# Optimization experiments

Measured on AMD Instinct MI355X. Metric: run time of the kernel, lower is better.

Reference implementation:

```python
import jax, jax.numpy as jnp
import numpy as np
from jax import lax

N = 1024          # proposals per image
C = 81            # classes incl. background
F = 1024          # feature dim
K = 100           # detections_per_img
IMG_W, IMG_H = 1216.0, 800.0
SCORE_THRESH = 0.05
NMS_THRESH = 0.5
BBOX_CLIP = float(np.log(1000.0 / 16.0))
WX, WY, WW, WH = 10.0, 10.0, 5.0, 5.0     # BoxCoder default weights


def setup_inputs() -> dict:
    key = jax.random.key(0)
    k1, k2, k3, k4, k5 = jax.random.split(key, 5)
    class_logits = jax.random.normal(k1, (N, C), jnp.float32) * 2.0
    box_regression = jax.random.normal(k2, (N, C * 4), jnp.float32) * 0.2
    xy = jax.random.uniform(k3, (N, 2), jnp.float32) * jnp.array([IMG_W * 0.7, IMG_H * 0.7], jnp.float32)
    wh = 16.0 + jax.random.uniform(k4, (N, 2), jnp.float32) * jnp.array([IMG_W * 0.3, IMG_H * 0.3], jnp.float32)
    proposal_boxes = jnp.concatenate([xy, xy + wh], axis=1)  # valid xyxy
    features = jax.random.normal(k5, (N, F), jnp.float32)
    return {"class_logits": class_logits, "box_regression": box_regression,
            "proposal_boxes": proposal_boxes, "features": features}


def _decode(rel, boxes):
    # BoxCoder.decode with weights (10,10,5,5), TO_REMOVE=1. rel:[N,C*4] boxes:[N,4] -> [N,C,4]
    rel = rel.reshape(N, C, 4)
    widths = boxes[:, 2] - boxes[:, 0] + 1.0
    heights = boxes[:, 3] - boxes[:, 1] + 1.0
    ctr_x = boxes[:, 0] + 0.5 * widths
    ctr_y = boxes[:, 1] + 0.5 * heights
    dx = rel[..., 0] / WX
    dy = rel[..., 1] / WY
    dw = jnp.minimum(rel[..., 2] / WW, BBOX_CLIP)
    dh = jnp.minimum(rel[..., 3] / WH, BBOX_CLIP)
    pcx = dx * widths[:, None] + ctr_x[:, None]
    pcy = dy * heights[:, None] + ctr_y[:, None]
    pw = jnp.exp(dw) * widths[:, None]
    ph = jnp.exp(dh) * heights[:, None]
    return jnp.stack([pcx - 0.5 * pw, pcy - 0.5 * ph,
                      pcx + 0.5 * pw - 1.0, pcy + 0.5 * ph - 1.0], axis=-1)


def _clip(b):
    # clip_to_image with TO_REMOVE=1
    x1 = jnp.clip(b[..., 0], 0.0, IMG_W - 1.0)
    y1 = jnp.clip(b[..., 1], 0.0, IMG_H - 1.0)
    x2 = jnp.clip(b[..., 2], 0.0, IMG_W - 1.0)
    y2 = jnp.clip(b[..., 3], 0.0, IMG_H - 1.0)
    return jnp.stack([x1, y1, x2, y2], axis=-1)


def _nms_class(boxes_c, scores_c, valid_c):
    # Sequential hard NMS for one class with fixed shapes. Invalid (below score
    # thresh) boxes can neither be kept nor suppress others.
    s_sort = jnp.where(valid_c, scores_c, -jnp.inf)
    order = jnp.argsort(-s_sort)              # descending score
    b = boxes_c[order]
    v = valid_c[order]
    s = scores_c[order]
    area = (b[:, 2] - b[:, 0] + 1.0) * (b[:, 3] - b[:, 1] + 1.0)
    lt = jnp.maximum(b[:, None, :2], b[None, :, :2])
    rb = jnp.minimum(b[:, None, 2:], b[None, :, 2:])
    whd = jnp.clip(rb - lt + 1.0, 0.0)
    inter = whd[..., 0] * whd[..., 1]
    iou = inter / (area[:, None] + area[None, :] - inter)  # [N,N]
    idx = jnp.arange(N)
    def body(i, keep):
        sup = (iou[i] > NMS_THRESH) & keep[i] & (idx > i)
        return keep & ~sup
    keep = lax.fori_loop(0, N, body, v)
    return b, order, jnp.where(keep, s, -1.0)


def reference(class_logits, box_regression, proposal_boxes, features):
    probs = jax.nn.softmax(class_logits, axis=-1)          # [N,C]
    dec = _clip(_decode(box_regression, proposal_boxes))    # [N,C,4]
    boxes_cls = jnp.transpose(dec[:, 1:, :], (1, 0, 2))     # [C-1,N,4] (skip background)
    scores_cls = probs[:, 1:].T                             # [C-1,N]
    valid = scores_cls > SCORE_THRESH
    b_s, order, s_kept = jax.vmap(_nms_class)(boxes_cls, scores_cls, valid)
    flat_s = s_kept.reshape(-1)                             # [(C-1)*N]
    top_s, top_i = lax.top_k(flat_s, K)
    cls_i = top_i // N
    pos_i = top_i % N
    boxes_out = b_s[cls_i, pos_i]                           # [K,4]
    orig = order[cls_i, pos_i]                              # original proposal idx
    feat_out = features[orig]                               # [K,F]
    labels = cls_i + 1
    ok = top_s > 0.0
    scores_out = jnp.where(ok, top_s, 0.0)
    boxes_out = jnp.where(ok[:, None], boxes_out, 0.0)
    feat_out = jnp.where(ok[:, None], feat_out, 0.0)
    labels = jnp.where(ok, labels, 0)
    return boxes_out, scores_out, feat_out, labels
```

## Files before the change

### kernel.cpp

```cpp
#include <hip/hip_runtime.h>
#include <math.h>

#define N 1024
#define C 81
#define F 1024
#define K 100
#define NC1 80
#define MAXC (NC1 * N)
#define HBASE 0x3D00
#define HSIZE 1024
#define SELCAP 2048

#define SCORE_THRESH 0.05f
#define NMS_THRESH   0.5f
#define BBOX_CLIP    4.135166556742356f
#define IMG_W1       1215.0f
#define IMG_H1       799.0f

typedef unsigned long long u64;
typedef unsigned int u32;

__device__ float4 decode_box(const float* __restrict__ pboxes,
                             const float* __restrict__ boxreg, int idx, int cl)
{
    float4 pb = ((const float4*)pboxes)[idx];
    float4 r  = *(const float4*)(boxreg + (size_t)idx * (C * 4) + cl * 4);
    float w  = pb.z - pb.x + 1.0f, h = pb.w - pb.y + 1.0f;
    float cx = pb.x + 0.5f * w,  cy = pb.y + 0.5f * h;
    float dx = r.x / 10.0f, dy = r.y / 10.0f;
    float dw = fminf(r.z / 5.0f, BBOX_CLIP);
    float dh = fminf(r.w / 5.0f, BBOX_CLIP);
    float pcx = dx * w + cx, pcy = dy * h + cy;
    float pw = expf(dw) * w, ph = expf(dh) * h;
    float x1 = pcx - 0.5f * pw,        y1 = pcy - 0.5f * ph;
    float x2 = pcx + 0.5f * pw - 1.0f, y2 = pcy + 0.5f * ph - 1.0f;
    x1 = fminf(fmaxf(x1, 0.0f), IMG_W1);
    y1 = fminf(fmaxf(y1, 0.0f), IMG_H1);
    x2 = fminf(fmaxf(x2, 0.0f), IMG_W1);
    y2 = fminf(fmaxf(y2, 0.0f), IMG_H1);
    return make_float4(x1, y1, x2, y2);
}

__global__ __launch_bounds__(256) void k_softmax(
    const float* __restrict__ logits, float2* __restrict__ ms,
    int* __restrict__ hist, int* __restrict__ counter)
{
    int gid = blockIdx.x * 256 + threadIdx.x;
    if (gid < HSIZE) hist[gid] = 0;
    if (gid == 0) *counter = 0;

    int n = blockIdx.x * 4 + (threadIdx.x >> 6);
    int t = threadIdx.x & 63;

    float v1 = logits[n * C + t];
    float v2 = (t < C - 64) ? logits[n * C + 64 + t] : -INFINITY;
    float m = fmaxf(v1, v2);
    for (int off = 32; off; off >>= 1) m = fmaxf(m, __shfl_xor(m, off));
    float e1 = expf(v1 - m);
    float e2 = (t < C - 64) ? expf(v2 - m) : 0.0f;
    float s = e1 + e2;
    for (int off = 32; off; off >>= 1) s += __shfl_xor(s, off);

    if (t == 0) ms[n] = make_float2(m, s);
}

__global__ __launch_bounds__(256) void k_class(
    const float* __restrict__ logits, const float* __restrict__ boxreg,
    const float* __restrict__ pboxes, const float2* __restrict__ ms,
    u64* __restrict__ ckey, float4* __restrict__ cbox, int* __restrict__ corig,
    int* __restrict__ hist, int* __restrict__ counter)
{
    int c = blockIdx.x;
    int cl = c + 1;
    int t = threadIdx.x;
    int lane = t & 63, wv = t >> 6;

    __shared__ u64    skey64[N];
    __shared__ float4 sbox[N];
    __shared__ float  sarea[N];
    __shared__ int    skeep[N];
    __shared__ u64    sup[256][4];
    __shared__ u64    skw[4];
    __shared__ int    swc[4];

    float2 p0 = ms[t],       p1 = ms[t + 256];
    float2 p2 = ms[t + 512], p3 = ms[t + 768];
    float s0 = expf(logits[(t      ) * C + cl] - p0.x) / p0.y;
    float s1 = expf(logits[(t + 256) * C + cl] - p1.x) / p1.y;
    float s2 = expf(logits[(t + 512) * C + cl] - p2.x) / p2.y;
    float s3 = expf(logits[(t + 768) * C + cl] - p3.x) / p3.y;
    int f0 = s0 > SCORE_THRESH, f1 = s1 > SCORE_THRESH;
    int f2 = s2 > SCORE_THRESH, f3 = s3 > SCORE_THRESH;

    u64 lmask = (1ull << lane) - 1ull;
    u64 b0 = __ballot(f0), b1 = __ballot(f1);
    u64 b2 = __ballot(f2), b3 = __ballot(f3);
    int wcount = __popcll(b0) + __popcll(b1) + __popcll(b2) + __popcll(b3);
    if (lane == 0) swc[wv] = wcount;
    __syncthreads();
    int w0c = swc[0], w1c = swc[1], w2c = swc[2], w3c = swc[3];
    int V = w0c + w1c + w2c + w3c;
    int wbase = (wv > 0 ? w0c : 0) + (wv > 1 ? w1c : 0) + (wv > 2 ? w2c : 0);
    {
        int o0 = wbase;
        int o1 = o0 + __popcll(b0);
        int o2 = o1 + __popcll(b1);
        int o3 = o2 + __popcll(b2);
        if (f0) skey64[o0 + __popcll(b0 & lmask)] =
            ((u64)__float_as_uint(s0) << 32) | (u32)~(u32)(t);
        if (f1) skey64[o1 + __popcll(b1 & lmask)] =
            ((u64)__float_as_uint(s1) << 32) | (u32)~(u32)(t + 256);
        if (f2) skey64[o2 + __popcll(b2 & lmask)] =
            ((u64)__float_as_uint(s2) << 32) | (u32)~(u32)(t + 512);
        if (f3) skey64[o3 + __popcll(b3 & lmask)] =
            ((u64)__float_as_uint(s3) << 32) | (u32)~(u32)(t + 768);
    }
    __syncthreads();
    if (V == 0) return;

    if (V <= 64) {
        if (t < 64) {
            u64 key = (lane < V) ? skey64[lane] : 0ull;
            for (int k = 2; k <= 64; k <<= 1) {
                for (int j = k >> 1; j > 0; j >>= 1) {
                    u64 other = __shfl_xor(key, j);
                    bool takeMax = (((lane & j) == 0) == ((lane & k) == 0));
                    bool gt = key > other;
                    key = (takeMax == gt) ? key : other;
                }
            }
            bool act = key != 0ull;
            float4 b = make_float4(0.f, 0.f, 0.f, 0.f);
            float area = 0.0f;
            if (act) {
                int idx = (int)(~(u32)(key & 0xffffffffu));
                b = decode_box(pboxes, boxreg, idx, cl);
                area = (b.z - b.x + 1.0f) * (b.w - b.y + 1.0f);
                cbox[c * N + lane]  = b;
                corig[c * N + lane] = idx;
            }
            int kept = act ? 1 : 0;
            for (int i = 0; i + 1 < V; ++i) {
                int   ki  = __shfl(kept, i);
                float bix = __shfl(b.x, i), biy = __shfl(b.y, i);
                float biz = __shfl(b.z, i), biw = __shfl(b.w, i);
                float ai  = __shfl(area, i);
                if (ki && lane > i && kept) {
                    float lx = fmaxf(bix, b.x), ly = fmaxf(biy, b.y);
                    float rx = fminf(biz, b.z), ry = fminf(biw, b.w);
                    float ww = fmaxf(rx - lx + 1.0f, 0.0f);
                    float hh = fmaxf(ry - ly + 1.0f, 0.0f);
                    float inter = ww * hh;
                    float iou = inter / (ai + area - inter);
                    if (iou > NMS_THRESH) kept = 0;
                }
            }
            if (kept) {
                int pos = atomicAdd(counter, 1);
                u32 sb = (u32)(key >> 32);
                ckey[pos] = ((u64)sb << 32) | (u64)(u32)~(u32)(c * N + lane);
                atomicAdd(&hist[(int)(sb >> 16) - HBASE], 1);
            }
        }
        return;
    }

    if (V <= 256) {
        int P = 128;
        while (P < V) P <<= 1;
        for (int i = V + t; i < P; i += 256) skey64[i] = 0ull;
        __syncthreads();
        for (int k = 2; k <= P; k <<= 1) {
            for (int j = k >> 1; j > 0; j >>= 1) {
                if (t < P) {
                    int i = t, ixj = i ^ j;
                    if (ixj > i) {
                        u64 a = skey64[i], bb = skey64[ixj];
                        bool desc = ((i & k) == 0);
                        if (desc ? (a < bb) : (a > bb)) { skey64[i] = bb; skey64[ixj] = a; }
                    }
                }
                __syncthreads();
            }
        }
        for (int p = t; p < V; p += 256) {
            int idx = (int)(~(u32)(skey64[p] & 0xffffffffu));
            float4 b = decode_box(pboxes, boxreg, idx, cl);
            sbox[p]  = b;
            sarea[p] = (b.z - b.x + 1.0f) * (b.w - b.y + 1.0f);
            cbox[c * N + p]  = b;
            corig[c * N + p] = idx;
        }
        __syncthreads();
        for (int i = t; i < V; i += 256) {
            float4 bi = sbox[i];
            float  ai = sarea[i];
            u64 w[4] = {0ull, 0ull, 0ull, 0ull};
            #pragma unroll
            for (int g = 0; g < 4; ++g) {
                int jlo = (i + 1 > g * 64) ? i + 1 : g * 64;
                int jhi = (V < (g + 1) * 64) ? V : (g + 1) * 64;
                for (int j = jlo; j < jhi; ++j) {
                    float4 bj = sbox[j];
                    float lx = fmaxf(bi.x, bj.x), ly = fmaxf(bi.y, bj.y);
                    float rx = fminf(bi.z, bj.z), ry = fminf(bi.w, bj.w);
                    float ww = fmaxf(rx - lx + 1.0f, 0.0f);
                    float hh = fmaxf(ry - ly + 1.0f, 0.0f);
                    float inter = ww * hh;
                    float iou = inter / (ai + sarea[j] - inter);
                    if (iou > NMS_THRESH) w[g] |= 1ull << (j & 63);
                }
            }
            sup[i][0] = w[0]; sup[i][1] = w[1];
            sup[i][2] = w[2]; sup[i][3] = w[3];
        }
        __syncthreads();
        if (t < 64) {
            u64 r0w0 = sup[t][0], r0w1 = sup[t][1], r0w2 = sup[t][2], r0w3 = sup[t][3];
            u64 r1w1 = 0, r1w2 = 0, r1w3 = 0;
            u64 r2w2 = 0, r2w3 = 0;
            u64 r3w3 = 0;
            if (64 + t < V)  { r1w1 = sup[64 + t][1];  r1w2 = sup[64 + t][2];  r1w3 = sup[64 + t][3]; }
            if (128 + t < V) { r2w2 = sup[128 + t][2]; r2w3 = sup[128 + t][3]; }
            if (192 + t < V) { r3w3 = sup[192 + t][3]; }
            u64 k0 = ~0ull, k1 = ~0ull, k2 = ~0ull, k3 = ~0ull;
            {
                int lim = (V < 64) ? V : 64;
                for (int i = 0; i < lim; ++i)
                    if ((k0 >> i) & 1) {
                        k0 &= ~__shfl(r0w0, i); k1 &= ~__shfl(r0w1, i);
                        k2 &= ~__shfl(r0w2, i); k3 &= ~__shfl(r0w3, i);
                    }
            }
            if (V > 64) {
                int lim = (V - 64 < 64) ? V - 64 : 64;
                for (int i = 0; i < lim; ++i)
                    if ((k1 >> i) & 1) {
                        k1 &= ~__shfl(r1w1, i);
                        k2 &= ~__shfl(r1w2, i); k3 &= ~__shfl(r1w3, i);
                    }
            }
            if (V > 128) {
                int lim = (V - 128 < 64) ? V - 128 : 64;
                for (int i = 0; i < lim; ++i)
                    if ((k2 >> i) & 1) {
                        k2 &= ~__shfl(r2w2, i); k3 &= ~__shfl(r2w3, i);
                    }
            }
            if (V > 192) {
                int lim = V - 192;
                for (int i = 0; i < lim; ++i)
                    if ((k3 >> i) & 1) k3 &= ~__shfl(r3w3, i);
            }
            if (t == 0) { skw[0] = k0; skw[1] = k1; skw[2] = k2; skw[3] = k3; }
        }
        __syncthreads();
        for (int p = t; p < V; p += 256) {
            if ((skw[p >> 6] >> (p & 63)) & 1ull) {
                int pos = atomicAdd(counter, 1);
                u32 sb = (u32)(skey64[p] >> 32);
                ckey[pos] = ((u64)sb << 32) | (u64)(u32)~(u32)(c * N + p);
                atomicAdd(&hist[(int)(sb >> 16) - HBASE], 1);
            }
        }
        return;
    }

    {
        int P = 512;
        while (P < V) P <<= 1;
        for (int i = V + t; i < P; i += 256) skey64[i] = 0ull;
        __syncthreads();
        for (int k = 2; k <= P; k <<= 1) {
            for (int j = k >> 1; j > 0; j >>= 1) {
                for (int i = t; i < P; i += 256) {
                    int ixj = i ^ j;
                    if (ixj > i) {
                        u64 a = skey64[i], bb = skey64[ixj];
                        bool desc = ((i & k) == 0);
                        if (desc ? (a < bb) : (a > bb)) { skey64[i] = bb; skey64[ixj] = a; }
                    }
                }
                __syncthreads();
            }
        }
        for (int p = t; p < V; p += 256) {
            int idx = (int)(~(u32)(skey64[p] & 0xffffffffu));
            float4 b = decode_box(pboxes, boxreg, idx, cl);
            sbox[p]  = b;
            sarea[p] = (b.z - b.x + 1.0f) * (b.w - b.y + 1.0f);
            skeep[p] = 1;
            cbox[c * N + p]  = b;
            corig[c * N + p] = idx;
        }
        __syncthreads();
        for (int i = 0; i < V; ++i) {
            if (skeep[i]) {
                float4 bi = sbox[i];
                float  ai = sarea[i];
                for (int j = i + 1 + t; j < V; j += 256) {
                    if (skeep[j]) {
                        float4 bj = sbox[j];
                        float lx = fmaxf(bi.x, bj.x), ly = fmaxf(bi.y, bj.y);
                        float rx = fminf(bi.z, bj.z), ry = fminf(bi.w, bj.w);
                        float ww = fmaxf(rx - lx + 1.0f, 0.0f);
                        float hh = fmaxf(ry - ly + 1.0f, 0.0f);
                        float inter = ww * hh;
                        float iou = inter / (ai + sarea[j] - inter);
                        if (iou > NMS_THRESH) skeep[j] = 0;
                    }
                }
            }
            __syncthreads();
        }
        for (int p = t; p < V; p += 256) {
            if (skeep[p]) {
                int pos = atomicAdd(counter, 1);
                u32 sb = (u32)(skey64[p] >> 32);
                ckey[pos] = ((u64)sb << 32) | (u64)(u32)~(u32)(c * N + p);
                atomicAdd(&hist[(int)(sb >> 16) - HBASE], 1);
            }
        }
    }
}

__global__ __launch_bounds__(1024) void k_select(
    const int* __restrict__ counter, u64* ckey, const int* __restrict__ hist,
    float* __restrict__ sel_score, int* __restrict__ sel_flat)
{
    int t = threadIdx.x;
    int lane = t & 63, wv = t >> 6;
    __shared__ u64 keys[SELCAP];
    __shared__ int swsum[16];
    __shared__ int sb_bstar, scount;
    __shared__ u64 wk[16];
    __shared__ int wp[16];

    int M = *counter;
    if (t == 0) { sb_bstar = 0; scount = 0; }

    int lsum = hist[t];
    int v = lsum;
    #pragma unroll
    for (int off = 1; off < 64; off <<= 1) {
        int o = __shfl_down(v, off);
        if (lane + off < 64) v += o;
    }
    if (lane == 0) swsum[wv] = v;
    __syncthreads();
    if (t < 64) {
        int w = (t < 16) ? swsum[t] : 0;
        #pragma unroll
        for (int off = 1; off < 16; off <<= 1) {
            int o = __shfl_down(w, off);
            if (t + off < 16) w += o;
        }
        if (t < 16) swsum[t] = w;
    }
    __syncthreads();
    int higher = (wv < 15) ? swsum[wv + 1] : 0;
    int base = v + higher - lsum;
    if (base < K && base + lsum >= K) sb_bstar = t;
    __syncthreads();
    int bstar = sb_bstar;

    for (int p = t; p < M; p += 1024) {
        u64 kk = ckey[p];
        int b = (int)((kk >> 48) & 0xFFFF) - HBASE;
        if (b >= bstar) {
            int pos = atomicAdd(&scount, 1);
            if (pos < SELCAP) keys[pos] = kk;
        }
    }
    __syncthreads();
    int cnt = scount;

    if (cnt > SELCAP) {
        for (int k = 0; k < K; ++k) {
            u64 key = 0ull; int pos = -1;
            for (int p = t; p < M; p += 1024) {
                u64 kk = ckey[p];
                if (kk > key) { key = kk; pos = p; }
            }
            for (int off = 32; off; off >>= 1) {
                u64 ok2 = __shfl_down(key, off);
                int op = __shfl_down(pos, off);
                if (ok2 > key) { key = ok2; pos = op; }
            }
            if ((t & 63) == 0) { wk[t >> 6] = key; wp[t >> 6] = pos; }
            __syncthreads();
            if (t == 0) {
                for (int w = 1; w < 16; ++w)
                    if (wk[w] > key) { key = wk[w]; pos = wp[w]; }
                if (key != 0ull) {
                    sel_score[k] = __uint_as_float((u32)(key >> 32));
                    sel_flat[k]  = (int)(~(u32)(key & 0xffffffffu));
                    ckey[pos] = 0ull;
                } else { sel_score[k] = 0.0f; sel_flat[k] = 0; }
            }
            __syncthreads();
        }
        return;
    }

    int P = 128;
    while (P < cnt) P <<= 1;
    for (int i = cnt + t; i < P; i += 1024) keys[i] = 0ull;
    __syncthreads();

    if (P <= 1024) {
        u64 key = (t < P) ? keys[t] : 0ull;
        for (int k = 2; k <= P; k <<= 1) {
            for (int j = k >> 1; j > 0; j >>= 1) {
                if (j >= 64) {
                    if (t < P) keys[t] = key;
                    __syncthreads();
                    if (t < P) {
                        u64 other = keys[t ^ j];
                        bool takeMax = (((t & j) == 0) == ((t & k) == 0));
                        bool gt = key > other;
                        key = (takeMax == gt) ? key : other;
                    }
                    __syncthreads();
                } else {
                    u64 other = __shfl_xor(key, j);
                    bool takeMax = (((t & j) == 0) == ((t & k) == 0));
                    bool gt = key > other;
                    if (t < P) key = (takeMax == gt) ? key : other;
                }
            }
        }
        if (t < K) {
            sel_score[t] = __uint_as_float((u32)(key >> 32));
            sel_flat[t]  = (int)(~(u32)(key & 0xffffffffu));
        }
        return;
    }

    for (int k = 2; k <= P; k <<= 1) {
        for (int j = k >> 1; j > 0; j >>= 1) {
            for (int i = t; i < P; i += 1024) {
                int ixj = i ^ j;
                if (ixj > i) {
                    u64 a = keys[i], b = keys[ixj];
                    bool desc = ((i & k) == 0);
                    if (desc ? (a < b) : (a > b)) { keys[i] = b; keys[ixj] = a; }
                }
            }
            __syncthreads();
        }
    }
    if (t < K) {
        u64 key = keys[t];
        sel_score[t] = __uint_as_float((u32)(key >> 32));
        sel_flat[t]  = (int)(~(u32)(key & 0xffffffffu));
    }
}

__global__ __launch_bounds__(256) void k_gather(
    const float* __restrict__ sel_score, const int* __restrict__ sel_flat,
    const int* __restrict__ corig, const float4* __restrict__ cbox,
    const float* __restrict__ feats, float* __restrict__ out)
{
    int k = blockIdx.x, t = threadIdx.x;
    float s = sel_score[k];
    bool ok = s > 0.0f;
    float4 b = make_float4(0.f, 0.f, 0.f, 0.f);
    int label = 0, orig = 0;
    if (ok) {
        int flat = sel_flat[k];
        orig  = corig[flat];
        b     = cbox[flat];
        label = (flat >> 10) + 1;
    }
    if (t == 0) {
        out[k * 4 + 0] = b.x; out[k * 4 + 1] = b.y;
        out[k * 4 + 2] = b.z; out[k * 4 + 3] = b.w;
        out[K * 4 + k] = ok ? s : 0.0f;
        out[K * 4 + K + K * F + k] = (float)label;
    }
    const float4* src = (const float4*)(feats + (size_t)orig * F);
    float4* dst = (float4*)(out + K * 4 + K + (size_t)k * F);
    float4 z = make_float4(0.f, 0.f, 0.f, 0.f);
    if (t < F / 4) dst[t] = ok ? src[t] : z;
}

extern "C" void kernel_launch(void* const* d_in, const int* in_sizes, int n_in,
                              void* d_out, int out_size, void* d_ws, size_t ws_size,
                              hipStream_t stream)
{
    const float* logits = (const float*)d_in[0];
    const float* boxreg = (const float*)d_in[1];
    const float* pboxes = (const float*)d_in[2];
    const float* feats  = (const float*)d_in[3];
    float* out = (float*)d_out;

    char* ws = (char*)d_ws;
    size_t off = 0;
    auto alloc = [&](size_t bytes) {
        size_t cur = off;
        off = (off + bytes + 255) & ~(size_t)255;
        return cur;
    };
    u64*    ckey      = (u64*)   (ws + alloc(sizeof(u64)    * MAXC));
    float4* cbox      = (float4*)(ws + alloc(sizeof(float4) * NC1 * N));
    int*    corig     = (int*)   (ws + alloc(sizeof(int)    * NC1 * N));
    float2* ms        = (float2*)(ws + alloc(sizeof(float2) * N));
    int*    hist      = (int*)   (ws + alloc(sizeof(int)    * HSIZE));
    int*    counter   = (int*)   (ws + alloc(sizeof(int)));
    float*  sel_score = (float*) (ws + alloc(sizeof(float)  * K));
    int*    sel_flat  = (int*)   (ws + alloc(sizeof(int)    * K));

    hipLaunchKernelGGL(k_softmax, dim3(N / 4), dim3(256), 0, stream,
                       logits, ms, hist, counter);
    hipLaunchKernelGGL(k_class, dim3(NC1), dim3(256), 0, stream,
                       logits, boxreg, pboxes, ms, ckey, cbox, corig, hist, counter);
    hipLaunchKernelGGL(k_select, dim3(1), dim3(1024), 0, stream,
                       counter, ckey, hist, sel_score, sel_flat);
    hipLaunchKernelGGL(k_gather, dim3(K), dim3(256), 0, stream,
                       sel_score, sel_flat, corig, cbox, feats, out);
}
```

Baseline: 96.80 us.

## Fuse per-class NMS, top-K select and gather into one last-block kernel

Merges the class NMS, global top-K selection and feature gather kernels into a single kernel. The last block to finish, detected with an atomic done counter and threadfence, performs the histogram threshold, the sort and the gather, which removes two kernel launches and their inter-kernel gaps. The mid-size class path now runs a register and shuffle bitonic sort instead of a shared-memory sort with a barrier per step. The trade-off is that selection and gather run on one 256-thread block instead of a 1024-thread block plus 100 gather blocks, so the tail is more serialized.

```diff
diff --git a/kernel.cpp b/kernel.cpp
--- a/kernel.cpp
+++ b/kernel.cpp
@@ -43,11 +43,11 @@
 
 __global__ __launch_bounds__(256) void k_softmax(
     const float* __restrict__ logits, float2* __restrict__ ms,
-    int* __restrict__ hist, int* __restrict__ counter)
+    int* __restrict__ hist, int* __restrict__ counter, int* __restrict__ done)
 {
     int gid = blockIdx.x * 256 + threadIdx.x;
     if (gid < HSIZE) hist[gid] = 0;
-    if (gid == 0) *counter = 0;
+    if (gid == 0) { *counter = 0; *done = 0; }
 
     int n = blockIdx.x * 4 + (threadIdx.x >> 6);
     int t = threadIdx.x & 63;
@@ -64,11 +64,13 @@
     if (t == 0) ms[n] = make_float2(m, s);
 }
 
-__global__ __launch_bounds__(256) void k_class(
+__global__ __launch_bounds__(256) void k_mega(
     const float* __restrict__ logits, const float* __restrict__ boxreg,
     const float* __restrict__ pboxes, const float2* __restrict__ ms,
+    const float* __restrict__ feats,
     u64* __restrict__ ckey, float4* __restrict__ cbox, int* __restrict__ corig,
-    int* __restrict__ hist, int* __restrict__ counter)
+    int* __restrict__ hist, int* __restrict__ counter, int* __restrict__ done,
+    float* __restrict__ out)
 {
     int c = blockIdx.x;
     int cl = c + 1;
@@ -82,6 +84,15 @@
     __shared__ u64    sup[256][4];
     __shared__ u64    skw[4];
     __shared__ int    swc[4];
+    __shared__ int    sLast;
+    __shared__ int    swsum4[4];
+    __shared__ int    sbstar, scount;
+    __shared__ u64    wk[4];
+    __shared__ int    wp[4];
+    __shared__ float  ssel_score[K];
+    __shared__ int    ssel_flat[K];
+    __shared__ int    sorig[K];
+    __shared__ int    sok[K];
 
     float2 p0 = ms[t],       p1 = ms[t + 256];
     float2 p2 = ms[t + 512], p3 = ms[t + 768];
@@ -116,9 +127,8 @@
             ((u64)__float_as_uint(s3) << 32) | (u32)~(u32)(t + 768);
     }
     __syncthreads();
-    if (V == 0) return;
-
-    if (V <= 64) {
+
+    if (V > 0 && V <= 64) {
         if (t < 64) {
             u64 key = (lane < V) ? skey64[lane] : 0ull;
             for (int k = 2; k <= 64; k <<= 1) {
@@ -162,37 +172,43 @@
                 atomicAdd(&hist[(int)(sb >> 16) - HBASE], 1);
             }
         }
-        return;
-    }
-
-    if (V <= 256) {
+    } else if (V > 64 && V <= 256) {
         int P = 128;
         while (P < V) P <<= 1;
-        for (int i = V + t; i < P; i += 256) skey64[i] = 0ull;
-        __syncthreads();
+        u64 key = (t < V) ? skey64[t] : 0ull;
         for (int k = 2; k <= P; k <<= 1) {
             for (int j = k >> 1; j > 0; j >>= 1) {
-                if (t < P) {
-                    int i = t, ixj = i ^ j;
-                    if (ixj > i) {
-                        u64 a = skey64[i], bb = skey64[ixj];
-                        bool desc = ((i & k) == 0);
-                        if (desc ? (a < bb) : (a > bb)) { skey64[i] = bb; skey64[ixj] = a; }
-                    }
-                }
-                __syncthreads();
-            }
-        }
-        for (int p = t; p < V; p += 256) {
-            int idx = (int)(~(u32)(skey64[p] & 0xffffffffu));
+                if (j >= 64) {
+                    if (t < P) skey64[t] = key;
+                    __syncthreads();
+                    if (t < P) {
+                        u64 other = skey64[t ^ j];
+                        bool takeMax = (((t & j) == 0) == ((t & k) == 0));
+                        bool gt = key > other;
+                        key = (takeMax == gt) ? key : other;
+                    }
+                    __syncthreads();
+                } else {
+                    u64 other = __shfl_xor(key, j);
+                    bool takeMax = (((t & j) == 0) == ((t & k) == 0));
+                    bool gt = key > other;
+                    if (t < P) key = (takeMax == gt) ? key : other;
+                }
+            }
+        }
+        if (t < P) skey64[t] = key;
+        __syncthreads();
+        if (t < V) {
+            int idx = (int)(~(u32)(skey64[t] & 0xffffffffu));
             float4 b = decode_box(pboxes, boxreg, idx, cl);
-            sbox[p]  = b;
-            sarea[p] = (b.z - b.x + 1.0f) * (b.w - b.y + 1.0f);
-            cbox[c * N + p]  = b;
-            corig[c * N + p] = idx;
-        }
-        __syncthreads();
-        for (int i = t; i < V; i += 256) {
+            sbox[t]  = b;
+            sarea[t] = (b.z - b.x + 1.0f) * (b.w - b.y + 1.0f);
+            cbox[c * N + t]  = b;
+            corig[c * N + t] = idx;
+        }
+        __syncthreads();
+        if (t < V) {
+            int i = t;
             float4 bi = sbox[i];
             float  ai = sarea[i];
             u64 w[4] = {0ull, 0ull, 0ull, 0ull};
@@ -255,18 +271,15 @@
             if (t == 0) { skw[0] = k0; skw[1] = k1; skw[2] = k2; skw[3] = k3; }
         }
         __syncthreads();
-        for (int p = t; p < V; p += 256) {
-            if ((skw[p >> 6] >> (p & 63)) & 1ull) {
+        if (t < V) {
+            if ((skw[t >> 6] >> (t & 63)) & 1ull) {
                 int pos = atomicAdd(counter, 1);
-                u32 sb = (u32)(skey64[p] >> 32);
-                ckey[pos] = ((u64)sb << 32) | (u64)(u32)~(u32)(c * N + p);
+                u32 sb = (u32)(skey64[t] >> 32);
+                ckey[pos] = ((u64)sb << 32) | (u64)(u32)~(u32)(c * N + t);
                 atomicAdd(&hist[(int)(sb >> 16) - HBASE], 1);
             }
         }
-        return;
-    }
-
-    {
+    } else if (V > 256) {
         int P = 512;
         while (P < V) P <<= 1;
         for (int i = V + t; i < P; i += 256) skey64[i] = 0ull;
@@ -322,167 +335,160 @@
             }
         }
     }
-}
-
-__global__ __launch_bounds__(1024) void k_select(
-    const int* __restrict__ counter, u64* ckey, const int* __restrict__ hist,
-    float* __restrict__ sel_score, int* __restrict__ sel_flat)
-{
-    int t = threadIdx.x;
-    int lane = t & 63, wv = t >> 6;
-    __shared__ u64 keys[SELCAP];
-    __shared__ int swsum[16];
-    __shared__ int sb_bstar, scount;
-    __shared__ u64 wk[16];
-    __shared__ int wp[16];
-
-    int M = *counter;
-    if (t == 0) { sb_bstar = 0; scount = 0; }
-
-    int lsum = hist[t];
-    int v = lsum;
-    #pragma unroll
-    for (int off = 1; off < 64; off <<= 1) {
-        int o = __shfl_down(v, off);
-        if (lane + off < 64) v += o;
-    }
-    if (lane == 0) swsum[wv] = v;
+
+    __threadfence();
     __syncthreads();
-    if (t < 64) {
-        int w = (t < 16) ? swsum[t] : 0;
+    if (t == 0) sLast = (atomicAdd(done, 1) == NC1 - 1);
+    __syncthreads();
+    if (!sLast) return;
+    __threadfence();
+
+    {
+        int M = *counter;
+        if (t == 0) { sbstar = 0; scount = 0; }
+
+        int h0 = hist[4 * t], h1 = hist[4 * t + 1];
+        int h2 = hist[4 * t + 2], h3 = hist[4 * t + 3];
+        int gs = h0 + h1 + h2 + h3;
+        int v = gs;
         #pragma unroll
-        for (int off = 1; off < 16; off <<= 1) {
-            int o = __shfl_down(w, off);
-            if (t + off < 16) w += o;
-        }
-        if (t < 16) swsum[t] = w;
+        for (int off = 1; off < 64; off <<= 1) {
+            int o = __shfl_down(v, off);
+            if (lane + off < 64) v += o;
+        }
+        if (lane == 0) swsum4[wv] = v;
+        __syncthreads();
+        int higher = 0;
+        for (int w = wv + 1; w < 4; ++w) higher += swsum4[w];
+        int above = v + higher - gs;
+        int b3 = above, b2 = b3 + h3, b1 = b2 + h2, b0 = b1 + h1;
+        if (b0 < K && b0 + h0 >= K) sbstar = 4 * t;
+        if (b1 < K && b1 + h1 >= K) sbstar = 4 * t + 1;
+        if (b2 < K && b2 + h2 >= K) sbstar = 4 * t + 2;
+        if (b3 < K && b3 + h3 >= K) sbstar = 4 * t + 3;
+        __syncthreads();
+        int bstar = sbstar;
+
+        u64* keys = (u64*)sbox;
+        for (int p = t; p < M; p += 256) {
+            u64 kk = ckey[p];
+            int b = (int)((kk >> 48) & 0xFFFF) - HBASE;
+            if (b >= bstar) {
+                int pos = atomicAdd(&scount, 1);
+                if (pos < SELCAP) keys[pos] = kk;
+            }
+        }
+        __syncthreads();
+        int cnt = scount;
+
+        if (cnt > SELCAP) {
+            for (int k = 0; k < K; ++k) {
+                u64 key = 0ull; int pos = -1;
+                for (int p = t; p < M; p += 256) {
+                    u64 kk = ckey[p];
+                    if (kk > key) { key = kk; pos = p; }
+                }
+                for (int off = 32; off; off >>= 1) {
+                    u64 ok2 = __shfl_down(key, off);
+                    int op  = __shfl_down(pos, off);
+                    if (ok2 > key) { key = ok2; pos = op; }
+                }
+                if ((t & 63) == 0) { wk[t >> 6] = key; wp[t >> 6] = pos; }
+                __syncthreads();
+                if (t == 0) {
+                    for (int w = 1; w < 4; ++w)
+                        if (wk[w] > key) { key = wk[w]; pos = wp[w]; }
+                    if (key != 0ull) {
+                        ssel_score[k] = __uint_as_float((u32)(key >> 32));
+                        ssel_flat[k]  = (int)(~(u32)(key & 0xffffffffu));
+                        ckey[pos] = 0ull;
+                    } else { ssel_score[k] = 0.0f; ssel_flat[k] = 0; }
+                }
+                __syncthreads();
+            }
+        } else {
+            int P = 128;
+            while (P < cnt) P <<= 1;
+            for (int i = cnt + t; i < P; i += 256) keys[i] = 0ull;
+            __syncthreads();
+            if (P <= 256) {
+                u64 key = (t < P) ? keys[t] : 0ull;
+                for (int k = 2; k <= P; k <<= 1) {
+                    for (int j = k >> 1; j > 0; j >>= 1) {
+                        if (j >= 64) {
+                            if (t < P) keys[t] = key;
+                            __syncthreads();
+                            if (t < P) {
+                                u64 other = keys[t ^ j];
+                                bool takeMax = (((t & j) == 0) == ((t & k) == 0));
+                                bool gt = key > other;
+                                key = (takeMax == gt) ? key : other;
+                            }
+                            __syncthreads();
+                        } else {
+                            u64 other = __shfl_xor(key, j);
+                            bool takeMax = (((t & j) == 0) == ((t & k) == 0));
+                            bool gt = key > other;
+                            if (t < P) key = (takeMax == gt) ? key : other;
+                        }
+                    }
+                }
+                if (t < K) {
+                    ssel_score[t] = __uint_as_float((u32)(key >> 32));
+                    ssel_flat[t]  = (int)(~(u32)(key & 0xffffffffu));
+                }
+            } else {
+                for (int k = 2; k <= P; k <<= 1) {
+                    for (int j = k >> 1; j > 0; j >>= 1) {
+                        for (int i = t; i < P; i += 256) {
+                            int ixj = i ^ j;
+                            if (ixj > i) {
+                                u64 a = keys[i], b = keys[ixj];
+                                bool desc = ((i & k) == 0);
+                                if (desc ? (a < b) : (a > b)) { keys[i] = b; keys[ixj] = a; }
+                            }
+                        }
+                        __syncthreads();
+                    }
+                }
+                if (t < K) {
+                    u64 key = keys[t];
+                    ssel_score[t] = __uint_as_float((u32)(key >> 32));
+                    ssel_flat[t]  = (int)(~(u32)(key & 0xffffffffu));
+                }
+            }
+        }
     }
     __syncthreads();
-    int higher = (wv < 15) ? swsum[wv + 1] : 0;
-    int base = v + higher - lsum;
-    if (base < K && base + lsum >= K) sb_bstar = t;
-    __syncthreads();
-    int bstar = sb_bstar;
-
-    for (int p = t; p < M; p += 1024) {
-        u64 kk = ckey[p];
-        int b = (int)((kk >> 48) & 0xFFFF) - HBASE;
-        if (b >= bstar) {
-            int pos = atomicAdd(&scount, 1);
-            if (pos < SELCAP) keys[pos] = kk;
-        }
+
+    if (t < K) {
+        float s = ssel_score[t];
+        bool ok = s > 0.0f;
+        float4 b = make_float4(0.f, 0.f, 0.f, 0.f);
+        int label = 0, orig = 0;
+        if (ok) {
+            int flat = ssel_flat[t];
+            orig  = corig[flat];
+            b     = cbox[flat];
+            label = (flat >> 10) + 1;
+        }
+        sorig[t] = orig;
+        sok[t]   = ok ? 1 : 0;
+        out[t * 4 + 0] = b.x; out[t * 4 + 1] = b.y;
+        out[t * 4 + 2] = b.z; out[t * 4 + 3] = b.w;
+        out[K * 4 + t] = ok ? s : 0.0f;
+        out[K * 4 + K + K * F + t] = (float)label;
     }
     __syncthreads();
-    int cnt = scount;
-
-    if (cnt > SELCAP) {
+    {
+        float4 z = make_float4(0.f, 0.f, 0.f, 0.f);
+        float4* dstbase = (float4*)(out + K * 4 + K);
+        #pragma unroll 2
         for (int k = 0; k < K; ++k) {
-            u64 key = 0ull; int pos = -1;
-            for (int p = t; p < M; p += 1024) {
-                u64 kk = ckey[p];
-                if (kk > key) { key = kk; pos = p; }
-            }
-            for (int off = 32; off; off >>= 1) {
-                u64 ok2 = __shfl_down(key, off);
-                int op = __shfl_down(pos, off);
-                if (ok2 > key) { key = ok2; pos = op; }
-            }
-            if ((t & 63) == 0) { wk[t >> 6] = key; wp[t >> 6] = pos; }
-            __syncthreads();
-            if (t == 0) {
-                for (int w = 1; w < 16; ++w)
-                    if (wk[w] > key) { key = wk[w]; pos = wp[w]; }
-                if (key != 0ull) {
-                    sel_score[k] = __uint_as_float((u32)(key >> 32));
-                    sel_flat[k]  = (int)(~(u32)(key & 0xffffffffu));
-                    ckey[pos] = 0ull;
-                } else { sel_score[k] = 0.0f; sel_flat[k] = 0; }
-            }
-            __syncthreads();
-        }
-        return;
+            const float4* src = (const float4*)(feats + (size_t)sorig[k] * F);
+            dstbase[(size_t)k * (F / 4) + t] = sok[k] ? src[t] : z;
+        }
     }
-
-    int P = 128;
-    while (P < cnt) P <<= 1;
-    for (int i = cnt + t; i < P; i += 1024) keys[i] = 0ull;
-    __syncthreads();
-
-    if (P <= 1024) {
-        u64 key = (t < P) ? keys[t] : 0ull;
-        for (int k = 2; k <= P; k <<= 1) {
-            for (int j = k >> 1; j > 0; j >>= 1) {
-                if (j >= 64) {
-                    if (t < P) keys[t] = key;
-                    __syncthreads();
-                    if (t < P) {
-                        u64 other = keys[t ^ j];
-                        bool takeMax = (((t & j) == 0) == ((t & k) == 0));
-                        bool gt = key > other;
-                        key = (takeMax == gt) ? key : other;
-                    }
-                    __syncthreads();
-                } else {
-                    u64 other = __shfl_xor(key, j);
-                    bool takeMax = (((t & j) == 0) == ((t & k) == 0));
-                    bool gt = key > other;
-                    if (t < P) key = (takeMax == gt) ? key : other;
-                }
-            }
-        }
-        if (t < K) {
-            sel_score[t] = __uint_as_float((u32)(key >> 32));
-            sel_flat[t]  = (int)(~(u32)(key & 0xffffffffu));
-        }
-        return;
-    }
-
-    for (int k = 2; k <= P; k <<= 1) {
-        for (int j = k >> 1; j > 0; j >>= 1) {
-            for (int i = t; i < P; i += 1024) {
-                int ixj = i ^ j;
-                if (ixj > i) {
-                    u64 a = keys[i], b = keys[ixj];
-                    bool desc = ((i & k) == 0);
-                    if (desc ? (a < b) : (a > b)) { keys[i] = b; keys[ixj] = a; }
-                }
-            }
-            __syncthreads();
-        }
-    }
-    if (t < K) {
-        u64 key = keys[t];
-        sel_score[t] = __uint_as_float((u32)(key >> 32));
-        sel_flat[t]  = (int)(~(u32)(key & 0xffffffffu));
-    }
-}
-
-__global__ __launch_bounds__(256) void k_gather(
-    const float* __restrict__ sel_score, const int* __restrict__ sel_flat,
-    const int* __restrict__ corig, const float4* __restrict__ cbox,
-    const float* __restrict__ feats, float* __restrict__ out)
-{
-    int k = blockIdx.x, t = threadIdx.x;
-    float s = sel_score[k];
-    bool ok = s > 0.0f;
-    float4 b = make_float4(0.f, 0.f, 0.f, 0.f);
-    int label = 0, orig = 0;
-    if (ok) {
-        int flat = sel_flat[k];
-        orig  = corig[flat];
-        b     = cbox[flat];
-        label = (flat >> 10) + 1;
-    }
-    if (t == 0) {
-        out[k * 4 + 0] = b.x; out[k * 4 + 1] = b.y;
-        out[k * 4 + 2] = b.z; out[k * 4 + 3] = b.w;
-        out[K * 4 + k] = ok ? s : 0.0f;
-        out[K * 4 + K + K * F + k] = (float)label;
-    }
-    const float4* src = (const float4*)(feats + (size_t)orig * F);
-    float4* dst = (float4*)(out + K * 4 + K + (size_t)k * F);
-    float4 z = make_float4(0.f, 0.f, 0.f, 0.f);
-    if (t < F / 4) dst[t] = ok ? src[t] : z;
 }
 
 extern "C" void kernel_launch(void* const* d_in, const int* in_sizes, int n_in,
@@ -508,15 +514,11 @@
     float2* ms        = (float2*)(ws + alloc(sizeof(float2) * N));
     int*    hist      = (int*)   (ws + alloc(sizeof(int)    * HSIZE));
     int*    counter   = (int*)   (ws + alloc(sizeof(int)));
-    float*  sel_score = (float*) (ws + alloc(sizeof(float)  * K));
-    int*    sel_flat  = (int*)   (ws + alloc(sizeof(int)    * K));
+    int*    done      = (int*)   (ws + alloc(sizeof(int)));
 
     hipLaunchKernelGGL(k_softmax, dim3(N / 4), dim3(256), 0, stream,
-                       logits, ms, hist, counter);
-    hipLaunchKernelGGL(k_class, dim3(NC1), dim3(256), 0, stream,
-                       logits, boxreg, pboxes, ms, ckey, cbox, corig, hist, counter);
-    hipLaunchKernelGGL(k_select, dim3(1), dim3(1024), 0, stream,
-                       counter, ckey, hist, sel_score, sel_flat);
-    hipLaunchKernelGGL(k_gather, dim3(K), dim3(256), 0, stream,
-                       sel_score, sel_flat, corig, cbox, feats, out);
+                       logits, ms, hist, counter, done);
+    hipLaunchKernelGGL(k_mega, dim3(NC1), dim3(256), 0, stream,
+                       logits, boxreg, pboxes, ms, feats,
+                       ckey, cbox, corig, hist, counter, done, out);
 }
```

After: 113.3 us. +17.1%, slower.
